# Optimization experiments

Measured on AMD Instinct MI355X. Metric: run time of the kernel, lower is better.

Reference implementation:

```python
import jax, jax.numpy as jnp
import numpy as np
import math

# Config (mirrors LlamaConfig passed to __init__)
V = 32000      # vocab_size
D = 1024       # n_embd
H = 16         # n_head
KVH = 4        # n_key_value_heads
R = H // KVH   # repeat_kv_heads = 4
HD = D // H    # head_size = 64
L = 4          # n_layer
I = 2730       # n_intermediate = 1024*4*2//3
T_CTX = 1024   # n_ctx / block_size
RD = HD        # rotary_dim = n_embd // n_head (full head rotated)
BASE = 10000.0 # rotary_base
EPS = 1e-6


def rope_sin_cos(T):
    # GPT-NeoX style (rotary_adjacent_pairs=False): freq repeated twice
    pos = jnp.arange(T, dtype=jnp.float32)
    dim = jnp.arange(RD // 2, dtype=jnp.float32)
    freq = BASE ** (dim / (RD / 2))
    freq = jnp.concatenate([freq, freq])          # (RD,)
    ang = pos[:, None] / freq[None, :]            # (T, RD)
    return jnp.sin(ang), jnp.cos(ang)


def apply_rope(x, sin, cos):
    # x: (B, H, T, HD); rotate_every_two with halves: [x0, x1] -> [-x1, x0]
    n = RD // 2
    flip = jnp.concatenate([-x[..., n:], x[..., :n]], axis=-1)
    return x * cos[None, None, :, :] + flip * sin[None, None, :, :]


def rmsnorm(x, w):
    xf = x.astype(jnp.float32)
    var = jnp.mean(xf * xf, axis=-1, keepdims=True)
    return w * (xf * jax.lax.rsqrt(var + EPS)).astype(x.dtype)


def attention(x, Wq, Wkv, Wo, sin, cos):
    B, T, C = x.shape
    kv = x @ Wkv.T                                 # (B, T, 2*C/R)
    k, v = jnp.split(kv, 2, axis=-1)               # each (B, T, KVH*HD)
    q = x @ Wq.T                                   # (B, T, C)
    # torch repeat_interleave(dim=1)+view(B,T,H,HD) == q head h reads kv head (h % KVH)
    k = jnp.tile(k.reshape(B, T, KVH, HD), (1, 1, R, 1)).transpose(0, 2, 1, 3)  # (B,H,T,HD)
    v = jnp.tile(v.reshape(B, T, KVH, HD), (1, 1, R, 1)).transpose(0, 2, 1, 3)
    q = q.reshape(B, T, H, HD).transpose(0, 2, 1, 3)
    q = apply_rope(q, sin, cos)
    k = apply_rope(k, sin, cos)
    scores = jnp.einsum('bhqd,bhkd->bhqk', q, k) * (1.0 / math.sqrt(HD))
    causal = jnp.tril(jnp.ones((T, T), dtype=bool))
    scores = jnp.where(causal[None, None], scores, -jnp.inf)
    att = jax.nn.softmax(scores, axis=-1)
    y = jnp.einsum('bhqk,bhkd->bhqd', att, v)
    y = y.transpose(0, 2, 1, 3).reshape(B, T, C)
    return y @ Wo.T


def swiglu(x, Wg, Wu, Wd):
    return (jax.nn.silu(x @ Wg.T) * (x @ Wu.T)) @ Wd.T


def setup_inputs() -> dict:
    key = jax.random.key(0)
    ks = jax.random.split(key, 10)
    std = 0.02
    res_std = 0.02 / math.sqrt(2 * L)  # LLMC_RESIDUAL_SCALE_FLAG projections
    wte = jax.random.normal(ks[0], (V, D), jnp.float32) * std
    Wq = jax.random.normal(ks[1], (L, D, D), jnp.float32) * std
    Wkv = jax.random.normal(ks[2], (L, 2 * D // R, D), jnp.float32) * std
    Wo = jax.random.normal(ks[3], (L, D, D), jnp.float32) * res_std
    Wg = jax.random.normal(ks[4], (L, I, D), jnp.float32) * std
    Wu = jax.random.normal(ks[5], (L, I, D), jnp.float32) * std
    Wd = jax.random.normal(ks[6], (L, D, I), jnp.float32) * res_std
    rms1 = jnp.ones((L, D), jnp.float32)
    rms2 = jnp.ones((L, D), jnp.float32)
    rms_f = jnp.ones((D,), jnp.float32)
    idx = jax.random.randint(ks[7], (2, 1024), 0, V, dtype=jnp.int64 if jax.config.jax_enable_x64 else jnp.int32)
    return dict(idx=idx, wte=wte, Wq=Wq, Wkv=Wkv, Wo=Wo, Wg=Wg, Wu=Wu, Wd=Wd,
                rms1=rms1, rms2=rms2, rms_f=rms_f)


def reference(idx, wte, Wq, Wkv, Wo, Wg, Wu, Wd, rms1, rms2, rms_f):
    B, T = idx.shape
    sin, cos = rope_sin_cos(T)
    x = wte[idx]                                   # (B, T, D)
    for l in range(L):
        x = x + attention(rmsnorm(x, rms1[l]), Wq[l], Wkv[l], Wo[l], sin, cos)
        x = x + swiglu(rmsnorm(x, rms2[l]), Wg[l], Wu[l], Wd[l])
    x = rmsnorm(x, rms_f)
    logits = x @ wte.T                             # tied lm_head
    return logits
```

## Files before the change

### kernel.cpp

```cpp
#include <hip/hip_runtime.h>
#include <hip/hip_bf16.h>
#include <math.h>

#define BB 2
#define TT 1024
#define DD 1024
#define NH 16
#define KVHN 4
#define NL 4
#define II 2730
#define IIP 2816
#define NTOK (BB * TT)
#define QKVD 1536
#define KSTR 72

typedef __hip_bfloat16 bf16;
typedef __attribute__((ext_vector_type(8))) short bf16x8;
typedef __attribute__((ext_vector_type(4))) float f32x4;

#define GLOAD16(gp, lp)                                                        \
    __builtin_amdgcn_global_load_lds(                                          \
        (const __attribute__((address_space(1))) unsigned int*)(gp),           \
        (__attribute__((address_space(3))) unsigned int*)(lp), 16, 0, 0)

__device__ inline float b2f(unsigned short u) {
    union { unsigned int i; float f; } v;
    v.i = (unsigned int)u << 16;
    return v.f;
}
__device__ inline unsigned short f2b(float f) {
    __hip_bfloat16 b = __float2bfloat16(f);
    return *(unsigned short*)&b;
}

__global__ void rope_table_k(float* __restrict__ st, float* __restrict__ ct) {
    int i = blockIdx.x * 256 + threadIdx.x;
    if (i >= TT * 64) return;
    int t = i >> 6, d = i & 63;
    float freq = powf(10000.0f, (float)(d & 31) / 32.0f);
    float ang = (float)t / freq;
    st[i] = sinf(ang);
    ct[i] = cosf(ang);
}

__global__ __launch_bounds__(256) void embed_k(const int* __restrict__ idx,
                                               const float* __restrict__ wte,
                                               float* __restrict__ x) {
    int row = blockIdx.x;
    int tok = idx[row];
    const float4* src = (const float4*)(wte + (size_t)tok * DD);
    float4* dst = (float4*)(x + (size_t)row * DD);
    dst[threadIdx.x] = src[threadIdx.x];
}

__global__ __launch_bounds__(256) void rmsnorm_k(const float* __restrict__ x,
                                                 const float* __restrict__ w,
                                                 bf16* __restrict__ o) {
    int row = blockIdx.x;
    float4 v = ((const float4*)(x + (size_t)row * DD))[threadIdx.x];
    float s = v.x * v.x + v.y * v.y + v.z * v.z + v.w * v.w;
#pragma unroll
    for (int off = 32; off > 0; off >>= 1) s += __shfl_down(s, off);
    __shared__ float red[4];
    if ((threadIdx.x & 63) == 0) red[threadIdx.x >> 6] = s;
    __syncthreads();
    float tot = red[0] + red[1] + red[2] + red[3];
    float r = rsqrtf(tot * (1.0f / DD) + 1e-6f);
    float4 wv = ((const float4*)w)[threadIdx.x];
    size_t base = (size_t)row * DD + threadIdx.x * 4;
    ushort4 ov;
    ov.x = f2b(v.x * r * wv.x);
    ov.y = f2b(v.y * r * wv.y);
    ov.z = f2b(v.z * r * wv.z);
    ov.w = f2b(v.w * r * wv.w);
    *(ushort4*)(o + base) = ov;
}

__global__ __launch_bounds__(256) void pack_v_k(const bf16* __restrict__ vb,
                                                bf16* __restrict__ vt) {
    int t0 = blockIdx.x * 64;
    int kvh = blockIdx.y;
    int b = blockIdx.z;
    __shared__ unsigned short Ls[64][65];
    int tid = threadIdx.x;
    const unsigned short* vbs = (const unsigned short*)vb;
    unsigned short* vts = (unsigned short*)vt;
    for (int e = tid; e < 64 * 64; e += 256) {
        int tl = e >> 6, d = e & 63;
        Ls[tl][d] = vbs[((size_t)(b * KVHN + kvh) * TT + t0 + tl) * 64 + d];
    }
    __syncthreads();
    for (int e = tid; e < 64 * 64; e += 256) {
        int d = e >> 6, tl = e & 63;
        vts[((size_t)(b * KVHN + kvh) * 64 + d) * TT + t0 + tl] = Ls[tl][d];
    }
}

__global__ __launch_bounds__(256) void attn_mfma_k(const bf16* __restrict__ qp,
                                                   const bf16* __restrict__ kp,
                                                   const bf16* __restrict__ vt,
                                                   bf16* __restrict__ y) {
    int qt = blockIdx.x;
    int h = blockIdx.y;
    int b = blockIdx.z;
    int kvh = h & (KVHN - 1);

    __shared__ __align__(16) bf16 Ks[64][KSTR];
    __shared__ __align__(16) bf16 Vt[64][KSTR];
    __shared__ __align__(16) bf16 Ps[4][16][KSTR];

    int tid = threadIdx.x;
    int lane = tid & 63;
    int w = tid >> 6;
    int qi = lane & 15;
    int g = lane >> 4;

    const bf16* qbase = qp + (((size_t)(b * NH + h) * TT + qt * 64 + w * 16 + qi) * 64);
    bf16x8 qf0 = *(const bf16x8*)(qbase + g * 8);
    bf16x8 qf1 = *(const bf16x8*)(qbase + 32 + g * 8);

    const bf16* kg = kp + ((size_t)(b * KVHN + kvh) * TT) * 64;
    const bf16* vg = vt + ((size_t)(b * KVHN + kvh) * 64) * TT;

    int c0 = tid, c1 = tid + 256;
    auto ldK = [&](int kt, int c) {
        return *(const bf16x8*)(kg + (size_t)(kt * 64 + (c >> 3)) * 64 + (c & 7) * 8);
    };
    auto ldV = [&](int kt, int c) {
        return *(const bf16x8*)(vg + (size_t)(c >> 3) * TT + kt * 64 + (c & 7) * 8);
    };

    f32x4 oacc[4] = {};
    float m = -INFINITY, l = 0.0f;
    int qglob = qt * 64 + w * 16 + qi;

    bf16x8 rk0 = ldK(0, c0), rk1 = ldK(0, c1);
    bf16x8 rv0 = ldV(0, c0), rv1 = ldV(0, c1);

    for (int kt = 0; kt <= qt; ++kt) {
        __syncthreads();
        *(bf16x8*)(&Ks[c0 >> 3][(c0 & 7) * 8]) = rk0;
        *(bf16x8*)(&Ks[c1 >> 3][(c1 & 7) * 8]) = rk1;
        *(bf16x8*)(&Vt[c0 >> 3][(c0 & 7) * 8]) = rv0;
        *(bf16x8*)(&Vt[c1 >> 3][(c1 & 7) * 8]) = rv1;
        __syncthreads();

        if (kt < qt) {
            rk0 = ldK(kt + 1, c0); rk1 = ldK(kt + 1, c1);
            rv0 = ldV(kt + 1, c0); rv1 = ldV(kt + 1, c1);
        }

        f32x4 sacc[4] = {};
#pragma unroll
        for (int stt = 0; stt < 4; ++stt) {
            bf16x8 kf0 = *(const bf16x8*)(&Ks[stt * 16 + qi][g * 8]);
            bf16x8 kf1 = *(const bf16x8*)(&Ks[stt * 16 + qi][32 + g * 8]);
            sacc[stt] = __builtin_amdgcn_mfma_f32_16x16x32_bf16(kf0, qf0, sacc[stt], 0, 0, 0);
            sacc[stt] = __builtin_amdgcn_mfma_f32_16x16x32_bf16(kf1, qf1, sacc[stt], 0, 0, 0);
        }

        if (kt == qt) {
#pragma unroll
            for (int stt = 0; stt < 4; ++stt)
#pragma unroll
                for (int r = 0; r < 4; ++r) {
                    int kgl = kt * 64 + stt * 16 + g * 4 + r;
                    if (kgl > qglob) sacc[stt][r] = -INFINITY;
                }
        }

        float tmax = -INFINITY;
#pragma unroll
        for (int stt = 0; stt < 4; ++stt)
#pragma unroll
            for (int r = 0; r < 4; ++r) tmax = fmaxf(tmax, sacc[stt][r]);
        tmax = fmaxf(tmax, __shfl_xor(tmax, 16));
        tmax = fmaxf(tmax, __shfl_xor(tmax, 32));
        float mnew = fmaxf(m, tmax);
        float scale = __expf(m - mnew);
        float psum = 0.0f;
#pragma unroll
        for (int stt = 0; stt < 4; ++stt) {
            bf16 pb[4];
#pragma unroll
            for (int r = 0; r < 4; ++r) {
                float p = __expf(sacc[stt][r] - mnew);
                psum += p;
                pb[r] = __float2bfloat16(p);
            }
            *(uint2*)(&Ps[w][qi][stt * 16 + g * 4]) = *(uint2*)pb;
        }
        psum += __shfl_xor(psum, 16);
        psum += __shfl_xor(psum, 32);
        l = l * scale + psum;
        m = mnew;

        float sc0 = __shfl(scale, g * 4 + 0);
        float sc1 = __shfl(scale, g * 4 + 1);
        float sc2 = __shfl(scale, g * 4 + 2);
        float sc3 = __shfl(scale, g * 4 + 3);
#pragma unroll
        for (int dt = 0; dt < 4; ++dt) {
            oacc[dt][0] *= sc0; oacc[dt][1] *= sc1;
            oacc[dt][2] *= sc2; oacc[dt][3] *= sc3;
        }

#pragma unroll
        for (int kc = 0; kc < 2; ++kc) {
            bf16x8 pa = *(const bf16x8*)(&Ps[w][qi][kc * 32 + g * 8]);
#pragma unroll
            for (int dt = 0; dt < 4; ++dt) {
                bf16x8 vb2 = *(const bf16x8*)(&Vt[dt * 16 + qi][kc * 32 + g * 8]);
                oacc[dt] = __builtin_amdgcn_mfma_f32_16x16x32_bf16(pa, vb2, oacc[dt], 0, 0, 0);
            }
        }
    }

    float linv = 1.0f / l;
    float li0 = __shfl(linv, g * 4 + 0);
    float li1 = __shfl(linv, g * 4 + 1);
    float li2 = __shfl(linv, g * 4 + 2);
    float li3 = __shfl(linv, g * 4 + 3);
#pragma unroll
    for (int dt = 0; dt < 4; ++dt) {
        int dcol = h * 64 + dt * 16 + qi;
        size_t r0 = (size_t)(b * TT + qt * 64 + w * 16 + g * 4) * DD + dcol;
        y[r0 + 0 * DD] = __float2bfloat16(oacc[dt][0] * li0);
        y[r0 + 1 * DD] = __float2bfloat16(oacc[dt][1] * li1);
        y[r0 + 2 * DD] = __float2bfloat16(oacc[dt][2] * li2);
        y[r0 + 3 * DD] = __float2bfloat16(oacc[dt][3] * li3);
    }
}

__device__ inline void cvt_one(const float* __restrict__ src, bf16* __restrict__ dst,
                               int Msrc, int Ksrc, int Kdst, int rmul, int radd,
                               int i4) {
    int i = i4 * 4;
    int r = i / Kdst, c = i - r * Kdst;
    ushort4 o;
    if (r < Msrc && c + 4 <= Ksrc && (Ksrc & 3) == 0) {
        float4 v = *(const float4*)(src + (size_t)r * Ksrc + c);
        o.x = f2b(v.x); o.y = f2b(v.y); o.z = f2b(v.z); o.w = f2b(v.w);
    } else {
        float v0 = (r < Msrc && c + 0 < Ksrc) ? src[(size_t)r * Ksrc + c + 0] : 0.0f;
        float v1 = (r < Msrc && c + 1 < Ksrc) ? src[(size_t)r * Ksrc + c + 1] : 0.0f;
        float v2 = (r < Msrc && c + 2 < Ksrc) ? src[(size_t)r * Ksrc + c + 2] : 0.0f;
        float v3 = (r < Msrc && c + 3 < Ksrc) ? src[(size_t)r * Ksrc + c + 3] : 0.0f;
        o.x = f2b(v0); o.y = f2b(v1); o.z = f2b(v2); o.w = f2b(v3);
    }
    *(ushort4*)(dst + ((size_t)(r * rmul + radd) * Kdst + c)) = o;
}

__global__ void cvt_pad_k(const float* __restrict__ src, bf16* __restrict__ dst,
                          int Msrc, int Ksrc, int Kdst, int total4) {
    for (int i4 = blockIdx.x * 256 + threadIdx.x; i4 < total4; i4 += gridDim.x * 256)
        cvt_one(src, dst, Msrc, Ksrc, Kdst, 1, 0, i4);
}

struct CvtJobs {
    const float* src[6];
    bf16* dst[6];
    int Msrc[6], Ksrc[6], Kdst[6], rmul[6], radd[6];
    int pfx[7];
};
__global__ void cvt_fused_k(CvtJobs j) {
    int total = j.pfx[6];
    for (int g = blockIdx.x * 256 + threadIdx.x; g < total; g += gridDim.x * 256) {
        int job = 0;
#pragma unroll
        for (int q = 1; q < 6; q++) job += (g >= j.pfx[q]) ? 1 : 0;
        int i4 = g - j.pfx[job];
        cvt_one(j.src[job], j.dst[job], j.Msrc[job], j.Ksrc[job], j.Kdst[job],
                j.rmul[job], j.radd[job], i4);
    }
}

template <int MODE, int BM, int BN>
__global__ __launch_bounds__(256) void gemm_bt(const bf16* __restrict__ A,
                                               const bf16* __restrict__ W16,
                                               const float* res, void* Cv,
                                               int N, int M, int K,
                                               const float* __restrict__ st,
                                               const float* __restrict__ ct,
                                               bf16* qp, bf16* kp, bf16* vb) {
    constexpr int MF = BM / 32;
    constexpr int NF = BN / 32;
    constexpr int ACH = BM / 32;
    constexpr int BCH = BN / 32;
    __shared__ __align__(16) bf16 As[BM * 64];
    __shared__ __align__(16) bf16 Bs[BN * 64];

    int t = threadIdx.x;
    int nnt = N / BM;
    int nmt = M / BN;
    int nwg = nmt * nnt;
    int orig = blockIdx.x;
    int q8 = nwg >> 3;
    int wgid = (orig & 7) * q8 + (orig >> 3);
    int mt, nt;
    if constexpr (BM == 128 && BN == 128) {
        int stile = wgid >> 5, rem = wgid & 31;
        mt = (stile << 1) + (rem & 1);
        nt = rem >> 1;
    } else {
        mt = wgid / nnt;
        nt = wgid - mt * nnt;
    }
    int m0 = mt * BN;
    int n0 = nt * BM;

    int lane = t & 63;
    int wave = t >> 6;
    int wr = (wave >> 1) * (BM / 2);
    int wc = (wave & 1) * (BN / 2);
    int qi = lane & 15;
    int g4 = lane >> 4;

    int arow[ACH], asc[ACH], apos[ACH];
#pragma unroll
    for (int i = 0; i < ACH; i++) {
        int p = (t + i * 256) * 16;
        arow[i] = p >> 7;
        asc[i] = (p & 127) ^ ((arow[i] & 7) << 4);
        apos[i] = p;
    }
    int brow[BCH], bsc[BCH], bpos[BCH];
#pragma unroll
    for (int i = 0; i < BCH; i++) {
        int p = (t + i * 256) * 16;
        brow[i] = p >> 7;
        bsc[i] = (p & 127) ^ ((brow[i] & 7) << 4);
        bpos[i] = p;
    }

    f32x4 acc[MF][NF] = {};

    for (int k0 = 0; k0 < K; k0 += 64) {
        __syncthreads();
#pragma unroll
        for (int i = 0; i < ACH; i++)
            GLOAD16(A + (size_t)(n0 + arow[i]) * K + k0 + (asc[i] >> 1),
                    (char*)As + apos[i]);
#pragma unroll
        for (int i = 0; i < BCH; i++)
            GLOAD16(W16 + (size_t)(m0 + brow[i]) * K + k0 + (bsc[i] >> 1),
                    (char*)Bs + bpos[i]);
        __syncthreads();

#pragma unroll
        for (int h = 0; h < 2; h++) {
            int cb = h * 64 + g4 * 16;
            bf16x8 af[MF], bfr[NF];
#pragma unroll
            for (int m = 0; m < MF; m++) {
                int r = wr + m * 16 + qi;
                af[m] = *(const bf16x8*)((const char*)As + r * 128 + (cb ^ ((r & 7) << 4)));
            }
#pragma unroll
            for (int n = 0; n < NF; n++) {
                int r = wc + n * 16 + qi;
                bfr[n] = *(const bf16x8*)((const char*)Bs + r * 128 + (cb ^ ((r & 7) << 4)));
            }
#pragma unroll
            for (int m = 0; m < MF; m++)
#pragma unroll
                for (int n = 0; n < NF; n++)
                    acc[m][n] = __builtin_amdgcn_mfma_f32_16x16x32_bf16(af[m], bfr[n], acc[m][n], 0, 0, 0);
        }
    }

    int colb = m0 + wc + qi;
    int rowb = n0 + wr + g4 * 4;

    if constexpr (MODE == 0) {
        float* Cf = (float*)Cv;
#pragma unroll
        for (int m = 0; m < MF; m++) {
#pragma unroll
            for (int n = 0; n < NF; n++) {
#pragma unroll
                for (int r = 0; r < 4; r++) {
                    size_t off = (size_t)(rowb + m * 16 + r) * M + (colb + n * 16);
                    __builtin_nontemporal_store(acc[m][n][r], Cf + off);
                }
            }
        }
    } else if constexpr (MODE == 1) {
        float* Cf = (float*)Cv;
#pragma unroll
        for (int m = 0; m < MF; m++) {
#pragma unroll
            for (int n = 0; n < NF; n++) {
#pragma unroll
                for (int r = 0; r < 4; r++) {
                    size_t off = (size_t)(rowb + m * 16 + r) * M + (colb + n * 16);
                    Cf[off] = acc[m][n][r] + res[off];
                }
            }
        }
    } else if constexpr (MODE == 3) {
        bf16* Cb = (bf16*)Cv;
        int M2 = M >> 1;
        bool even = (lane & 1) == 0;
#pragma unroll
        for (int m = 0; m < MF; m++) {
#pragma unroll
            for (int n = 0; n < NF; n++) {
#pragma unroll
                for (int r = 0; r < 4; r++) {
                    float own = acc[m][n][r];
                    float oth = __shfl_xor(own, 1);
                    if (even) {
                        float sv = own / (1.0f + __expf(-own)) * oth;
                        int oc = (colb + n * 16) >> 1;
                        Cb[(size_t)(rowb + m * 16 + r) * M2 + oc] = __float2bfloat16(sv);
                    }
                }
            }
        }
    } else if constexpr (MODE == 4) {
        int h = (m0 + wc) >> 6;
#pragma unroll
        for (int m = 0; m < MF; m++) {
#pragma unroll
            for (int r = 0; r < 4; r++) {
                int row = rowb + m * 16 + r;
                int tt = row & (TT - 1);
                int b = row >> 10;
                if (h < 20) {
#pragma unroll
                    for (int n = 0; n < 2; n++) {
                        int dlo = qi + n * 16;
                        float alo = acc[m][n][r];
                        float ahi = acc[m][n + 2][r];
                        float c = ct[tt * 64 + dlo];
                        float s = st[tt * 64 + dlo];
                        float olo = alo * c - ahi * s;
                        float ohi = ahi * c + alo * s;
                        if (h < 16) {
                            olo *= 0.125f; ohi *= 0.125f;
                            bf16* q = qp + (((size_t)(b * NH + h) * TT + tt) * 64);
                            q[dlo] = __float2bfloat16(olo);
                            q[dlo + 32] = __float2bfloat16(ohi);
                        } else {
                            bf16* kk = kp + (((size_t)(b * KVHN + (h - 16)) * TT + tt) * 64);
                            kk[dlo] = __float2bfloat16(olo);
                            kk[dlo + 32] = __float2bfloat16(ohi);
                        }
                    }
                } else {
                    bf16* vv = vb + (((size_t)(b * KVHN + (h - 20)) * TT + tt) * 64);
#pragma unroll
                    for (int n = 0; n < 4; n++)
                        vv[qi + n * 16] = __float2bfloat16(acc[m][n][r]);
                }
            }
        }
    }
}

extern "C" void kernel_launch(void* const* d_in, const int* in_sizes, int n_in,
                              void* d_out, int out_size, void* d_ws, size_t ws_size,
                              hipStream_t stream) {
    const int* idx    = (const int*)d_in[0];
    const float* wte  = (const float*)d_in[1];
    const float* Wq   = (const float*)d_in[2];
    const float* Wkv  = (const float*)d_in[3];
    const float* Wo   = (const float*)d_in[4];
    const float* Wg   = (const float*)d_in[5];
    const float* Wu   = (const float*)d_in[6];
    const float* Wd   = (const float*)d_in[7];
    const float* rms1 = (const float*)d_in[8];
    const float* rms2 = (const float*)d_in[9];
    const float* rmsf = (const float*)d_in[10];
    float* out = (float*)d_out;

    char* ws = (char*)d_ws;
    size_t off = 0;
    float* x = (float*)(ws + off);   off += (size_t)NTOK * DD * 4;
    bf16* xn = (bf16*)(ws + off);    off += (size_t)NTOK * DD * 2;
    float* st = (float*)(ws + off);  off += (size_t)TT * 64 * 4;
    float* ct = (float*)(ws + off);  off += (size_t)TT * 64 * 4;
    bf16* yb = (bf16*)(ws + off);    off += (size_t)NTOK * DD * 2;
    bf16* gb = (bf16*)(ws + off);    off += (size_t)NTOK * IIP * 2;
    bf16* qp = (bf16*)(ws + off);    off += (size_t)NTOK * DD * 2;
    bf16* kp = (bf16*)(ws + off);    off += (size_t)BB * KVHN * TT * 64 * 2;
    bf16* vb = (bf16*)(ws + off);    off += (size_t)BB * KVHN * TT * 64 * 2;
    bf16* vt = (bf16*)(ws + off);    off += (size_t)BB * KVHN * TT * 64 * 2;
    bf16* Wqkv_buf = (bf16*)(ws + off); off += (size_t)QKVD * DD * 2;
    bf16* Wo_buf = (bf16*)(ws + off);   off += (size_t)DD * DD * 2;
    bf16* Wgu_buf = (bf16*)(ws + off);  off += (size_t)2 * IIP * DD * 2;
    bf16* Wd_buf = (bf16*)(ws + off);   off += (size_t)DD * IIP * 2;
    bf16* wte_bf = (bf16*)(ws + off);   off += (size_t)32000 * DD * 2;

    rope_table_k<<<(TT * 64 + 255) / 256, 256, 0, stream>>>(st, ct);
    embed_k<<<NTOK, 256, 0, stream>>>(idx, wte, x);

    for (int l = 0; l < NL; ++l) {
        CvtJobs j;
        int n4[6];
        j.src[0] = Wq + (size_t)l * DD * DD;   j.dst[0] = Wqkv_buf;
        j.Msrc[0] = DD;  j.Ksrc[0] = DD;  j.Kdst[0] = DD;  n4[0] = DD * DD / 4;
        j.rmul[0] = 1; j.radd[0] = 0;
        j.src[1] = Wkv + (size_t)l * 512 * DD; j.dst[1] = Wqkv_buf + (size_t)DD * DD;
        j.Msrc[1] = 512; j.Ksrc[1] = DD;  j.Kdst[1] = DD;  n4[1] = 512 * DD / 4;
        j.rmul[1] = 1; j.radd[1] = 0;
        j.src[2] = Wo + (size_t)l * DD * DD;   j.dst[2] = Wo_buf;
        j.Msrc[2] = DD;  j.Ksrc[2] = DD;  j.Kdst[2] = DD;  n4[2] = DD * DD / 4;
        j.rmul[2] = 1; j.radd[2] = 0;
        j.src[3] = Wg + (size_t)l * II * DD;   j.dst[3] = Wgu_buf;
        j.Msrc[3] = II;  j.Ksrc[3] = DD;  j.Kdst[3] = DD;  n4[3] = IIP * DD / 4;
        j.rmul[3] = 2; j.radd[3] = 0;
        j.src[4] = Wu + (size_t)l * II * DD;   j.dst[4] = Wgu_buf;
        j.Msrc[4] = II;  j.Ksrc[4] = DD;  j.Kdst[4] = DD;  n4[4] = IIP * DD / 4;
        j.rmul[4] = 2; j.radd[4] = 1;
        j.src[5] = Wd + (size_t)l * DD * II;   j.dst[5] = Wd_buf;
        j.Msrc[5] = DD;  j.Ksrc[5] = II;  j.Kdst[5] = IIP; n4[5] = DD * IIP / 4;
        j.rmul[5] = 1; j.radd[5] = 0;
        j.pfx[0] = 0;
        for (int q = 0; q < 6; q++) j.pfx[q + 1] = j.pfx[q] + n4[q];
        cvt_fused_k<<<2048, 256, 0, stream>>>(j);

        rmsnorm_k<<<NTOK, 256, 0, stream>>>(x, rms1 + (size_t)l * DD, xn);
        gemm_bt<4, 64, 128><<<(QKVD / 128) * (NTOK / 64), 256, 0, stream>>>(
            xn, Wqkv_buf, nullptr, nullptr, NTOK, QKVD, DD, st, ct, qp, kp, vb);
        pack_v_k<<<dim3(TT / 64, KVHN, BB), 256, 0, stream>>>(vb, vt);
        attn_mfma_k<<<dim3(TT / 64, NH, BB), 256, 0, stream>>>(qp, kp, vt, yb);
        gemm_bt<1, 64, 64><<<(DD / 64) * (NTOK / 64), 256, 0, stream>>>(
            yb, Wo_buf, x, x, NTOK, DD, DD, nullptr, nullptr, nullptr, nullptr, nullptr);
        rmsnorm_k<<<NTOK, 256, 0, stream>>>(x, rms2 + (size_t)l * DD, xn);
        gemm_bt<3, 128, 128><<<(2 * IIP / 128) * (NTOK / 128), 256, 0, stream>>>(
            xn, Wgu_buf, nullptr, gb, NTOK, 2 * IIP, DD, nullptr, nullptr, nullptr, nullptr, nullptr);
        gemm_bt<1, 64, 64><<<(DD / 64) * (NTOK / 64), 256, 0, stream>>>(
            gb, Wd_buf, x, x, NTOK, DD, IIP, nullptr, nullptr, nullptr, nullptr, nullptr);
    }

    rmsnorm_k<<<NTOK, 256, 0, stream>>>(x, rmsf, xn);
    cvt_pad_k<<<2048, 256, 0, stream>>>(wte, wte_bf, 32000, DD, DD, 32000 * DD / 4);
    gemm_bt<0, 128, 64><<<(32000 / 64) * (NTOK / 128), 256, 0, stream>>>(
        xn, wte_bf, nullptr, out, NTOK, 32000, DD, nullptr, nullptr, nullptr, nullptr, nullptr);
}
```

Measured before the change: 849.4 us.

## Double-buffer LDS loads in the lm_head GEMM with async prefetch

```diff
diff --git a/kernel.cpp b/kernel.cpp
--- a/kernel.cpp
+++ b/kernel.cpp
@@ -275,7 +275,7 @@
     }
 }
 
-template <int MODE, int BM, int BN>
+template <int MODE, int BM, int BN, int DBUF = 0>
 __global__ __launch_bounds__(256) void gemm_bt(const bf16* __restrict__ A,
                                                const bf16* __restrict__ W16,
                                                const float* res, void* Cv,
@@ -287,8 +287,8 @@
     constexpr int NF = BN / 32;
     constexpr int ACH = BM / 32;
     constexpr int BCH = BN / 32;
-    __shared__ __align__(16) bf16 As[BM * 64];
-    __shared__ __align__(16) bf16 Bs[BN * 64];
+    __shared__ __align__(16) bf16 As[(DBUF ? 2 : 1) * BM * 64];
+    __shared__ __align__(16) bf16 Bs[(DBUF ? 2 : 1) * BN * 64];
 
     int t = threadIdx.x;
     int nnt = N / BM;
@@ -335,18 +335,7 @@
 
     f32x4 acc[MF][NF] = {};
 
-    for (int k0 = 0; k0 < K; k0 += 64) {
-        __syncthreads();
-#pragma unroll
-        for (int i = 0; i < ACH; i++)
-            GLOAD16(A + (size_t)(n0 + arow[i]) * K + k0 + (asc[i] >> 1),
-                    (char*)As + apos[i]);
-#pragma unroll
-        for (int i = 0; i < BCH; i++)
-            GLOAD16(W16 + (size_t)(m0 + brow[i]) * K + k0 + (bsc[i] >> 1),
-                    (char*)Bs + bpos[i]);
-        __syncthreads();
-
+    auto compute_step = [&](const char* Ab, const char* Bb) {
 #pragma unroll
         for (int h = 0; h < 2; h++) {
             int cb = h * 64 + g4 * 16;
@@ -354,18 +343,57 @@
 #pragma unroll
             for (int m = 0; m < MF; m++) {
                 int r = wr + m * 16 + qi;
-                af[m] = *(const bf16x8*)((const char*)As + r * 128 + (cb ^ ((r & 7) << 4)));
+                af[m] = *(const bf16x8*)(Ab + r * 128 + (cb ^ ((r & 7) << 4)));
             }
 #pragma unroll
             for (int n = 0; n < NF; n++) {
                 int r = wc + n * 16 + qi;
-                bfr[n] = *(const bf16x8*)((const char*)Bs + r * 128 + (cb ^ ((r & 7) << 4)));
+                bfr[n] = *(const bf16x8*)(Bb + r * 128 + (cb ^ ((r & 7) << 4)));
             }
 #pragma unroll
             for (int m = 0; m < MF; m++)
 #pragma unroll
                 for (int n = 0; n < NF; n++)
                     acc[m][n] = __builtin_amdgcn_mfma_f32_16x16x32_bf16(af[m], bfr[n], acc[m][n], 0, 0, 0);
+        }
+    };
+
+    if constexpr (DBUF) {
+        auto stage = [&](int k0, int buf) {
+            char* Ad = (char*)As + buf * (BM * 128);
+            char* Bd = (char*)Bs + buf * (BN * 128);
+#pragma unroll
+            for (int i = 0; i < ACH; i++)
+                GLOAD16(A + (size_t)(n0 + arow[i]) * K + k0 + (asc[i] >> 1), Ad + apos[i]);
+#pragma unroll
+            for (int i = 0; i < BCH; i++)
+                GLOAD16(W16 + (size_t)(m0 + brow[i]) * K + k0 + (bsc[i] >> 1), Bd + bpos[i]);
+        };
+        int NK = K >> 6;
+        stage(0, 0);
+        stage(64, 1);
+        for (int j = 0; j < NK; ++j) {
+            if (j < NK - 1) asm volatile("s_waitcnt vmcnt(6)" ::: "memory");
+            else            asm volatile("s_waitcnt vmcnt(0)" ::: "memory");
+            __builtin_amdgcn_s_barrier();
+            compute_step((const char*)As + (j & 1) * (BM * 128),
+                         (const char*)Bs + (j & 1) * (BN * 128));
+            __builtin_amdgcn_s_barrier();
+            if (j + 2 < NK) stage((j + 2) << 6, j & 1);
+        }
+    } else {
+        for (int k0 = 0; k0 < K; k0 += 64) {
+            __syncthreads();
+#pragma unroll
+            for (int i = 0; i < ACH; i++)
+                GLOAD16(A + (size_t)(n0 + arow[i]) * K + k0 + (asc[i] >> 1),
+                        (char*)As + apos[i]);
+#pragma unroll
+            for (int i = 0; i < BCH; i++)
+                GLOAD16(W16 + (size_t)(m0 + brow[i]) * K + k0 + (bsc[i] >> 1),
+                        (char*)Bs + bpos[i]);
+            __syncthreads();
+            compute_step((const char*)As, (const char*)Bs);
         }
     }
 
@@ -537,6 +565,6 @@
 
     rmsnorm_k<<<NTOK, 256, 0, stream>>>(x, rmsf, xn);
     cvt_pad_k<<<2048, 256, 0, stream>>>(wte, wte_bf, 32000, DD, DD, 32000 * DD / 4);
-    gemm_bt<0, 128, 64><<<(32000 / 64) * (NTOK / 128), 256, 0, stream>>>(
+    gemm_bt<0, 128, 64, 1><<<(32000 / 64) * (NTOK / 128), 256, 0, stream>>>(
         xn, wte_bf, nullptr, out, NTOK, 32000, DD, nullptr, nullptr, nullptr, nullptr, nullptr);
 }
```

After: 833.0 us. No clear change (-1.9%).
